# Performance work log

Hardware: AMD Instinct MI355X
Metric: run time of the kernel (lower is better)

Reference implementation:

```python
import jax, jax.numpy as jnp
import numpy as np

N, D_IN, D, E, B = 30000, 512, 512, 300000, 4096
N_RES, N_DNN = 2, 2
EPS = 1e-5


def _ln(x, g, b):
    mu = jnp.mean(x, axis=-1, keepdims=True)
    var = jnp.mean((x - mu) ** 2, axis=-1, keepdims=True)
    return (x - mu) * jax.lax.rsqrt(var + EPS) * g + b


def setup_inputs() -> dict:
    key = jax.random.key(0)
    ks = jax.random.split(key, 16)
    s = 1.0 / np.sqrt(D)
    inp = {
        "node_feat": jax.random.normal(ks[0], (N, D_IN), jnp.float32),
        "edge_hop0": jax.random.randint(ks[1], (2, E), 0, N, jnp.int32),
        "edge_hop1": jax.random.randint(ks[2], (2, E), 0, N, jnp.int32),
        "target_idx": jax.random.randint(ks[3], (B,), 0, N, jnp.int32),
        # node transform
        "Wt": jax.random.normal(ks[4], (D_IN, D), jnp.float32) / np.sqrt(D_IN),
        "bt": jnp.zeros((D,), jnp.float32),
        # GATConv (shared across both hops, one relation)
        "Wf": jax.random.normal(ks[5], (D, D), jnp.float32) * s,
        "bf": jnp.zeros((D,), jnp.float32),
        "w_att": jax.random.normal(ks[6], (2 * D,), jnp.float32) * s,
        "b_att": jnp.zeros((), jnp.float32),
        "gat_bias": jnp.zeros((D,), jnp.float32),
        # Res_DNN
        "Wp": jax.random.normal(ks[7], (D, D), jnp.float32) * s,
        "bp": jnp.zeros((D,), jnp.float32),
        "dnn_W": jax.random.normal(ks[8], (N_RES, N_DNN, D, D), jnp.float32) * s,
        "dnn_b": jnp.zeros((N_RES, N_DNN, D), jnp.float32),
        "dnn_g": jnp.ones((N_RES, N_DNN, D), jnp.float32),
        "dnn_beta": jnp.zeros((N_RES, N_DNN, D), jnp.float32),
        "res_g": jnp.ones((N_RES, D), jnp.float32),
        "res_beta": jnp.zeros((N_RES, D), jnp.float32),
        "Wc": jax.random.normal(ks[9], (D, 1), jnp.float32) * s,
        "bc": jnp.zeros((1,), jnp.float32),
    }
    return inp


def _gat(feat, edges, Wf, bf, w_att, b_att, gat_bias):
    # dst and src are the same node set / same features here
    h = feat @ Wf + bf                      # [N, D]
    di, si = edges[0], edges[1]             # [E], [E]
    # att(concat(dst_h, src_h)) == dst_h @ w[:D] + src_h @ w[D:] + b
    sd = h @ w_att[:D]                      # [N]
    ss = h @ w_att[D:]                      # [N]
    e = jnp.tanh(sd[di] + ss[si] + b_att)   # [E]
    # sparse softmax per destination row
    m = jax.ops.segment_max(e, di, num_segments=N)
    a = jnp.exp(e - m[di])
    denom = jax.ops.segment_sum(a, di, num_segments=N)
    alpha = a / denom[di]                   # [E]
    # sparse-mm aggregation
    out = jax.ops.segment_sum(alpha[:, None] * h[si], di, num_segments=N)
    return out + gat_bias


def reference(node_feat, edge_hop0, edge_hop1, target_idx, Wt, bt, Wf, bf,
              w_att, b_att, gat_bias, Wp, bp, dnn_W, dnn_b, dnn_g, dnn_beta,
              res_g, res_beta, Wc, bc):
    # node-type feature transform (dropout is identity at inference)
    feat = node_feat @ Wt + bt              # [N, D]
    # hops processed from last to first: hop1 then hop0
    for edges in (edge_hop1, edge_hop0):
        g = _gat(feat, edges, Wf, bf, w_att, b_att, gat_bias)
        feat = (feat + g) * 0.5             # mean of stacked [orig, gat_out]
    h = feat[target_idx]                    # [B, D]
    # Res_DNN head
    h = h @ Wp + bp
    for r in range(N_RES):
        sc = h
        for i in range(N_DNN):
            h = _ln(jnp.tanh(h @ dnn_W[r, i] + dnn_b[r, i]), dnn_g[r, i], dnn_beta[r, i])
        h = _ln(jnp.tanh(sc + h), res_g[r], res_beta[r])
    logits = h @ Wc + bc                    # [B, 1]
    return jax.nn.sigmoid(logits)
```

## Files before the change

### kernel.cpp

```cpp
#include <hip/hip_runtime.h>

#define D 512
typedef unsigned short ushort_t;
typedef __attribute__((ext_vector_type(8))) short bf16x8;
typedef __attribute__((ext_vector_type(4))) float f32x4;

static __device__ __forceinline__ ushort_t f2bf(float f) {
  unsigned u = __float_as_uint(f);
  u += 0x7fffu + ((u >> 16) & 1u);
  return (ushort_t)(u >> 16);
}
static __device__ __forceinline__ float bf2f(ushort_t h) {
  return __uint_as_float(((unsigned)h) << 16);
}

static __device__ __forceinline__ void gld_lds16(const void* g, void* lds) {
  __builtin_amdgcn_global_load_lds(
      (const __attribute__((address_space(1))) unsigned int*)g,
      (__attribute__((address_space(3))) unsigned int*)lds, 16, 0, 0);
}

__global__ __launch_bounds__(256) void pack_weight(
    const float* __restrict__ W, ushort_t* __restrict__ out, int K, int N, int nmat) {
  int i = blockIdx.x * 256 + threadIdx.x;
  const int per = K * N;
  if (i >= per * nmat) return;
  const int mat = i / per;
  const int r = i - mat * per;
  const int k = r / N, n = r - k * N;
  const int nt = n >> 4, col = n & 15, kt = k >> 5, kg = (k >> 3) & 3, j = k & 7;
  out[(size_t)mat * per + (((size_t)nt * (K >> 5) + kt) << 9) + ((kg << 4) + col) * 8 + j] =
      f2bf(W[(size_t)mat * per + r]);
}

__global__ __launch_bounds__(256) void conv_bf16_pad(
    const float* __restrict__ in, ushort_t* __restrict__ out, int M, int Mp, int K) {
  const size_t i4 = ((size_t)blockIdx.x * 256 + threadIdx.x) * 4;
  if (i4 >= (size_t)Mp * K) return;
  const int row = (int)(i4 / K);
  ushort4 o;
  if (row < M) {
    const float4 v = *reinterpret_cast<const float4*>(&in[i4]);
    o.x = f2bf(v.x); o.y = f2bf(v.y); o.z = f2bf(v.z); o.w = f2bf(v.w);
  } else {
    o.x = o.y = o.z = o.w = 0;
  }
  *reinterpret_cast<ushort4*>(&out[i4]) = o;
}

__global__ __launch_bounds__(512) void gemm_mfma(
    const ushort_t* __restrict__ A, const ushort_t* __restrict__ Bp,
    const float* __restrict__ bias, ushort_t* __restrict__ C16,
    const float* __restrict__ watt, float* __restrict__ sd_part,
    float* __restrict__ ss_part, int Mp, int N, int K) {
  __shared__ __align__(16) ushort_t As[2][8 * 512];
  __shared__ __align__(16) ushort_t Bs[2][8 * 512];
  const int nwg = gridDim.x;
  const int q = nwg >> 3, rm = nwg & 7;
  const int xcd = blockIdx.x & 7, kk = blockIdx.x >> 3;
  const int lin = (xcd < rm ? xcd * (q + 1) : rm * (q + 1) + (xcd - rm) * q) + kk;
  const int m0 = (lin >> 2) * 128;
  const int n0 = (lin & 3) * 128;
  const int tid = threadIdx.x;
  const int lane = tid & 63;
  const int wid = tid >> 6;
  const int wm = wid >> 1;
  const int wn = wid & 1;
  const int arow = lane & 15;
  const int akoff = (lane >> 4) * 8;
  const int c15 = lane & 15;
  const int rgrp = lane >> 4;
  const int kt32 = K >> 5;
  f32x4 acc[2][4] = {};

  auto stage = [&](int kt, int b) {
    const int k0 = kt * 32;
    gld_lds16(&A[(size_t)(m0 + wid * 16 + arow) * K + k0 + akoff],
              &As[b][wid * 512]);
    gld_lds16(&Bp[(((size_t)(n0 / 16 + wid) * kt32 + kt) << 9) + lane * 8],
              &Bs[b][wid * 512]);
  };

  stage(0, 0);
  __syncthreads();
  int cur = 0;
  for (int t = 0; t < kt32; ++t) {
    if (t + 1 < kt32) stage(t + 1, cur ^ 1);
    bf16x8 af[2], bfr[4];
#pragma unroll
    for (int mi = 0; mi < 2; ++mi)
      af[mi] = *reinterpret_cast<const bf16x8*>(&As[cur][(wm * 2 + mi) * 512 + lane * 8]);
#pragma unroll
    for (int ni = 0; ni < 4; ++ni)
      bfr[ni] = *reinterpret_cast<const bf16x8*>(&Bs[cur][(wn * 4 + ni) * 512 + lane * 8]);
#pragma unroll
    for (int mi = 0; mi < 2; ++mi)
#pragma unroll
      for (int ni = 0; ni < 4; ++ni)
        acc[mi][ni] = __builtin_amdgcn_mfma_f32_16x16x32_bf16(af[mi], bfr[ni], acc[mi][ni], 0, 0, 0);
    __syncthreads();
    cur ^= 1;
  }
  const int band = (n0 >> 6) + wn;
#pragma unroll
  for (int mi = 0; mi < 2; ++mi) {
    const int row = m0 + wm * 32 + mi * 16 + (rgrp << 2);
#pragma unroll
    for (int r = 0; r < 4; ++r) {
      float psd = 0.f, pss = 0.f;
#pragma unroll
      for (int ni = 0; ni < 4; ++ni) {
        const int col = n0 + wn * 64 + ni * 16 + c15;
        const float v = acc[mi][ni][r] + bias[col];
        C16[(size_t)(row + r) * N + col] = f2bf(v);
        if (watt) {
          psd += v * watt[col];
          pss += v * watt[D + col];
        }
      }
      if (watt) {
#pragma unroll
        for (int off = 8; off > 0; off >>= 1) {
          psd += __shfl_xor(psd, off);
          pss += __shfl_xor(pss, off);
        }
        if (c15 == 0) {
          sd_part[(size_t)band * Mp + row + r] = psd;
          ss_part[(size_t)band * Mp + row + r] = pss;
        }
      }
    }
  }
}

__global__ __launch_bounds__(256) void combine_dots(
    const float* __restrict__ sd_part, const float* __restrict__ ss_part,
    float* __restrict__ sd, float* __restrict__ ss, int Mp, int Nn) {
  const int i = blockIdx.x * 256 + threadIdx.x;
  if (i >= Nn) return;
  float a = 0.f, b = 0.f;
#pragma unroll
  for (int bnd = 0; bnd < 8; ++bnd) {
    a += sd_part[(size_t)bnd * Mp + i];
    b += ss_part[(size_t)bnd * Mp + i];
  }
  sd[i] = a;
  ss[i] = b;
}

__global__ void fill_bucket(const int* __restrict__ e1, const int* __restrict__ e0,
                            int* __restrict__ cnt, int* __restrict__ bucket,
                            int Nn, int E) {
  const int e = blockIdx.x * blockDim.x + threadIdx.x;
  if (e >= E) return;
  const int d1 = e1[e];
  const int p1 = atomicAdd(&cnt[d1], 1);
  if (p1 < 64) bucket[(size_t)d1 * 64 + p1] = e1[E + e];
  const int d0 = e0[e];
  const int p0 = atomicAdd(&cnt[Nn + d0], 1);
  if (p0 < 64) bucket[((size_t)(Nn + d0)) * 64 + p0] = e0[E + e];
}

__global__ __launch_bounds__(256) void gat_aggregate_w(
    ushort_t* __restrict__ featb, const ushort_t* __restrict__ hb,
    const float* __restrict__ sd, const float* __restrict__ ss,
    const int* __restrict__ di, const int* __restrict__ si,
    const float* __restrict__ b_att_p, const float* __restrict__ gat_bias,
    const int* __restrict__ cnt, const int* __restrict__ bucket, int Nn, int E) {
  const int dst = blockIdx.x * 4 + (threadIdx.x >> 6);
  const int lane = threadIdx.x & 63;
  if (dst >= Nn) return;
  const int deg = cnt[dst];
  const float sdd = sd[dst];
  const float ba = b_att_p[0];
  const size_t o = (size_t)dst * D + lane * 8;
  bf16x8 fv = *reinterpret_cast<const bf16x8*>(&featb[o]);
  float acc[8] = {};
  if (deg <= 64) {
    const bool valid = lane < deg;
    const int slane = valid ? bucket[(size_t)dst * 64 + lane] : 0;
    const float e = valid ? tanhf(sdd + ss[slane] + ba) : -1e30f;
    float m = e;
#pragma unroll
    for (int off = 32; off > 0; off >>= 1) m = fmaxf(m, __shfl_xor(m, off));
    const float a = valid ? expf(e - m) : 0.f;
    float s = a;
#pragma unroll
    for (int off = 32; off > 0; off >>= 1) s += __shfl_xor(s, off);
    const float w = a * ((s > 0.f) ? 1.f / s : 0.f);
    int k = 0;
    for (; k + 3 < deg; k += 4) {
      const float w0 = __shfl(w, k), w1 = __shfl(w, k + 1);
      const float w2 = __shfl(w, k + 2), w3 = __shfl(w, k + 3);
      const int s0 = __shfl(slane, k), s1 = __shfl(slane, k + 1);
      const int s2 = __shfl(slane, k + 2), s3 = __shfl(slane, k + 3);
      const bf16x8 h0 = *reinterpret_cast<const bf16x8*>(&hb[(size_t)s0 * D + lane * 8]);
      const bf16x8 h1 = *reinterpret_cast<const bf16x8*>(&hb[(size_t)s1 * D + lane * 8]);
      const bf16x8 h2 = *reinterpret_cast<const bf16x8*>(&hb[(size_t)s2 * D + lane * 8]);
      const bf16x8 h3 = *reinterpret_cast<const bf16x8*>(&hb[(size_t)s3 * D + lane * 8]);
#pragma unroll
      for (int qq = 0; qq < 8; ++qq) {
        const float t0 = w0 * bf2f((ushort_t)h0[qq]) + w1 * bf2f((ushort_t)h1[qq]);
        const float t1 = w2 * bf2f((ushort_t)h2[qq]) + w3 * bf2f((ushort_t)h3[qq]);
        acc[qq] += t0 + t1;
      }
    }
    for (; k < deg; ++k) {
      const float wk = __shfl(w, k);
      const int sk = __shfl(slane, k);
      const bf16x8 h0 = *reinterpret_cast<const bf16x8*>(&hb[(size_t)sk * D + lane * 8]);
#pragma unroll
      for (int qq = 0; qq < 8; ++qq) acc[qq] += wk * bf2f((ushort_t)h0[qq]);
    }
  } else {
    float m = -1e30f;
    for (int e = lane; e < E; e += 64)
      if (di[e] == dst) m = fmaxf(m, tanhf(sdd + ss[si[e]] + ba));
#pragma unroll
    for (int off = 32; off > 0; off >>= 1) m = fmaxf(m, __shfl_xor(m, off));
    float s = 0.f;
    for (int e = lane; e < E; e += 64)
      if (di[e] == dst) s += expf(tanhf(sdd + ss[si[e]] + ba) - m);
#pragma unroll
    for (int off = 32; off > 0; off >>= 1) s += __shfl_xor(s, off);
    const float inv = (s > 0.f) ? 1.f / s : 0.f;
    for (int base = 0; base < E; base += 64) {
      const int e = base + lane;
      const bool hit = (e < E) && (di[e] == dst);
      unsigned long long mask = __ballot(hit);
      const int sidx = hit ? si[e] : 0;
      const float aval = hit ? expf(tanhf(sdd + ss[sidx] + ba) - m) * inv : 0.f;
      while (mask) {
        const int l = __ffsll((long long)mask) - 1;
        mask &= mask - 1;
        const float wv = __shfl(aval, l);
        const int sk = __shfl(sidx, l);
        const bf16x8 hv = *reinterpret_cast<const bf16x8*>(&hb[(size_t)sk * D + lane * 8]);
#pragma unroll
        for (int qq = 0; qq < 8; ++qq) acc[qq] += wv * bf2f((ushort_t)hv[qq]);
      }
    }
  }
#pragma unroll
  for (int q = 0; q < 8; ++q) {
    const float f = (bf2f((ushort_t)fv[q]) + acc[q] + gat_bias[lane * 8 + q]) * 0.5f;
    fv[q] = (short)f2bf(f);
  }
  *reinterpret_cast<bf16x8*>(&featb[o]) = fv;
}

__global__ __launch_bounds__(1024, 4) void head_fused(
    const ushort_t* __restrict__ featb, const int* __restrict__ tidx,
    const ushort_t* __restrict__ pWp, const float* __restrict__ bp,
    const ushort_t* __restrict__ pDW, const float* __restrict__ dnn_b,
    const float* __restrict__ dnn_g, const float* __restrict__ dnn_be,
    const float* __restrict__ res_g, const float* __restrict__ res_be,
    const float* __restrict__ Wc, const float* __restrict__ bc,
    float* __restrict__ out) {
  __shared__ __align__(16) ushort_t A_lds[16 * 512];
  __shared__ float lsum[16][16], lsq[16][16], meanv[16], rsv[16];
  const int tid = threadIdx.x;
  const int lane = tid & 63;
  const int wave = tid >> 6;
  const int nt0 = wave * 2;
  const int c15 = lane & 15;
  const int rgrp = lane >> 4;

  {
    const int row = tid >> 6, col8 = tid & 63;
    const int g = tidx[blockIdx.x * 16 + row];
    const bf16x8 v = *reinterpret_cast<const bf16x8*>(&featb[(size_t)g * D + col8 * 8]);
    *reinterpret_cast<bf16x8*>(&A_lds[row * 512 + (col8 ^ (row & 7)) * 8]) = v;
  }
  __syncthreads();

  auto do_gemm = [&](const ushort_t* __restrict__ W, f32x4& a0, f32x4& a1) {
    a0 = f32x4{0.f, 0.f, 0.f, 0.f};
    a1 = f32x4{0.f, 0.f, 0.f, 0.f};
    bf16x8 c0 = *reinterpret_cast<const bf16x8*>(
        &W[(((size_t)nt0 * 16 + 0) << 9) + lane * 8]);
    bf16x8 c1 = *reinterpret_cast<const bf16x8*>(
        &W[(((size_t)(nt0 + 1) * 16 + 0) << 9) + lane * 8]);
#pragma unroll
    for (int kt = 0; kt < 16; ++kt) {
      bf16x8 n0 = c0, n1 = c1;
      if (kt < 15) {
        n0 = *reinterpret_cast<const bf16x8*>(
            &W[(((size_t)nt0 * 16 + kt + 1) << 9) + lane * 8]);
        n1 = *reinterpret_cast<const bf16x8*>(
            &W[(((size_t)(nt0 + 1) * 16 + kt + 1) << 9) + lane * 8]);
      }
      const int col8 = kt * 4 + rgrp;
      const bf16x8 af = *reinterpret_cast<const bf16x8*>(
          &A_lds[c15 * 512 + (col8 ^ (c15 & 7)) * 8]);
      a0 = __builtin_amdgcn_mfma_f32_16x16x32_bf16(af, c0, a0, 0, 0, 0);
      a1 = __builtin_amdgcn_mfma_f32_16x16x32_bf16(af, c1, a1, 0, 0, 0);
      c0 = n0;
      c1 = n1;
    }
  };

  auto block_ln = [&](f32x4& v0, f32x4& v1, const float* __restrict__ g,
                      const float* __restrict__ be) {
    float psum[4], psq[4];
#pragma unroll
    for (int r = 0; r < 4; ++r) {
      psum[r] = v0[r] + v1[r];
      psq[r] = v0[r] * v0[r] + v1[r] * v1[r];
    }
#pragma unroll
    for (int off = 8; off > 0; off >>= 1)
#pragma unroll
      for (int r = 0; r < 4; ++r) {
        psum[r] += __shfl_xor(psum[r], off);
        psq[r] += __shfl_xor(psq[r], off);
      }
    if (c15 == 0) {
#pragma unroll
      for (int r = 0; r < 4; ++r) {
        lsum[wave][rgrp * 4 + r] = psum[r];
        lsq[wave][rgrp * 4 + r] = psq[r];
      }
    }
    __syncthreads();
    if (tid < 16) {
      float s = 0.f, qq = 0.f;
#pragma unroll
      for (int w = 0; w < 16; ++w) { s += lsum[w][tid]; qq += lsq[w][tid]; }
      const float mean = s * (1.f / 512.f);
      const float var = qq * (1.f / 512.f) - mean * mean;
      meanv[tid] = mean;
      rsv[tid] = rsqrtf(var + 1e-5f);
    }
    __syncthreads();
    const int col0 = nt0 * 16 + c15;
    const int col1 = (nt0 + 1) * 16 + c15;
    const float g0 = g[col0], b0 = be[col0];
    const float g1 = g[col1], b1 = be[col1];
#pragma unroll
    for (int r = 0; r < 4; ++r) {
      const int row = rgrp * 4 + r;
      v0[r] = (v0[r] - meanv[row]) * rsv[row] * g0 + b0;
      v1[r] = (v1[r] - meanv[row]) * rsv[row] * g1 + b1;
    }
  };

  auto store_A = [&](const f32x4& v0, const f32x4& v1) {
    const int col0 = nt0 * 16 + c15;
    const int col1 = (nt0 + 1) * 16 + c15;
#pragma unroll
    for (int r = 0; r < 4; ++r) {
      const int row = rgrp * 4 + r;
      A_lds[row * 512 + (((col0 >> 3) ^ (row & 7)) << 3) + (col0 & 7)] = f2bf(v0[r]);
      A_lds[row * 512 + (((col1 >> 3) ^ (row & 7)) << 3) + (col1 & 7)] = f2bf(v1[r]);
    }
  };

  f32x4 sc0, sc1, acc0, acc1, ln0, ln1;

  do_gemm(pWp, acc0, acc1);
  {
    const float bv0 = bp[nt0 * 16 + c15];
    const float bv1 = bp[(nt0 + 1) * 16 + c15];
#pragma unroll
    for (int r = 0; r < 4; ++r) { sc0[r] = acc0[r] + bv0; sc1[r] = acc1[r] + bv1; }
  }
  __syncthreads();
  store_A(sc0, sc1);
  __syncthreads();

  for (int rb = 0; rb < 2; ++rb) {
    {
      const int st = rb * 2;
      do_gemm(pDW + (size_t)st * D * D, acc0, acc1);
      const float bv0 = dnn_b[st * D + nt0 * 16 + c15];
      const float bv1 = dnn_b[st * D + (nt0 + 1) * 16 + c15];
#pragma unroll
      for (int r = 0; r < 4; ++r) {
        acc0[r] = tanhf(acc0[r] + bv0);
        acc1[r] = tanhf(acc1[r] + bv1);
      }
      block_ln(acc0, acc1, dnn_g + st * D, dnn_be + st * D);
      store_A(acc0, acc1);
      __syncthreads();
    }
    {
      const int st = rb * 2 + 1;
      do_gemm(pDW + (size_t)st * D * D, ln0, ln1);
      const float bv0 = dnn_b[st * D + nt0 * 16 + c15];
      const float bv1 = dnn_b[st * D + (nt0 + 1) * 16 + c15];
#pragma unroll
      for (int r = 0; r < 4; ++r) {
        ln0[r] = tanhf(ln0[r] + bv0);
        ln1[r] = tanhf(ln1[r] + bv1);
      }
      block_ln(ln0, ln1, dnn_g + st * D, dnn_be + st * D);
    }
#pragma unroll
    for (int r = 0; r < 4; ++r) {
      acc0[r] = tanhf(sc0[r] + ln0[r]);
      acc1[r] = tanhf(sc1[r] + ln1[r]);
    }
    block_ln(acc0, acc1, res_g + rb * D, res_be + rb * D);
    sc0 = acc0;
    sc1 = acc1;
    if (rb == 0) {
      store_A(sc0, sc1);
      __syncthreads();
    }
  }

  float pr[4];
  {
    const float w0 = Wc[nt0 * 16 + c15];
    const float w1 = Wc[(nt0 + 1) * 16 + c15];
#pragma unroll
    for (int r = 0; r < 4; ++r) pr[r] = sc0[r] * w0 + sc1[r] * w1;
  }
#pragma unroll
  for (int off = 8; off > 0; off >>= 1)
#pragma unroll
    for (int r = 0; r < 4; ++r) pr[r] += __shfl_xor(pr[r], off);
  __syncthreads();
  if (c15 == 0) {
#pragma unroll
    for (int r = 0; r < 4; ++r) lsum[wave][rgrp * 4 + r] = pr[r];
  }
  __syncthreads();
  if (tid < 16) {
    float s = 0.f;
#pragma unroll
    for (int w = 0; w < 16; ++w) s += lsum[w][tid];
    out[blockIdx.x * 16 + tid] = 1.f / (1.f + expf(-(s + bc[0])));
  }
}

extern "C" void kernel_launch(void* const* d_in, const int* in_sizes, int n_in,
                              void* d_out, int out_size, void* d_ws, size_t ws_size,
                              hipStream_t stream) {
  (void)n_in; (void)out_size; (void)ws_size;
  const float* node_feat = (const float*)d_in[0];
  const int* edge0 = (const int*)d_in[1];
  const int* edge1 = (const int*)d_in[2];
  const int* tidx = (const int*)d_in[3];
  const float* Wt = (const float*)d_in[4];
  const float* bt = (const float*)d_in[5];
  const float* Wf = (const float*)d_in[6];
  const float* bfp = (const float*)d_in[7];
  const float* w_att = (const float*)d_in[8];
  const float* b_att = (const float*)d_in[9];
  const float* gat_bias = (const float*)d_in[10];
  const float* Wp = (const float*)d_in[11];
  const float* bp = (const float*)d_in[12];
  const float* dnn_W = (const float*)d_in[13];
  const float* dnn_b = (const float*)d_in[14];
  const float* dnn_g = (const float*)d_in[15];
  const float* dnn_be = (const float*)d_in[16];
  const float* res_g = (const float*)d_in[17];
  const float* res_be = (const float*)d_in[18];
  const float* Wc = (const float*)d_in[19];
  const float* bc = (const float*)d_in[20];
  float* out = (float*)d_out;

  const int Nn = in_sizes[0] / D;
  const int E = in_sizes[1] / 2;
  const int B = in_sizes[3];
  const int K_IN = in_sizes[4] / D;
  const int Mp = (Nn + 127) / 128 * 128;
  const int N2 = 2 * Nn;

  char* p = (char*)d_ws;
  auto alloc = [&](size_t bytes) -> char* {
    char* r = p;
    p += (bytes + 255) & ~(size_t)255;
    return r;
  };
  ushort_t* featb = (ushort_t*)alloc((size_t)Mp * D * 2);
  ushort_t* hb = (ushort_t*)alloc((size_t)Mp * D * 2);
  float* sd = (float*)alloc((size_t)Nn * 4);
  float* ss = (float*)alloc((size_t)Nn * 4);
  float* sd_part = (float*)alloc((size_t)8 * Mp * 4);
  float* ss_part = (float*)alloc((size_t)8 * Mp * 4);
  int* cnt = (int*)alloc((size_t)N2 * 4);
  int* bucket = (int*)alloc((size_t)N2 * 64 * 4);
  ushort_t* pWt = (ushort_t*)alloc((size_t)K_IN * D * 2);
  ushort_t* pWf = (ushort_t*)alloc((size_t)D * D * 2);
  ushort_t* pWp = (ushort_t*)alloc((size_t)D * D * 2);
  ushort_t* pDWall = (ushort_t*)alloc((size_t)4 * D * D * 2);

  dim3 blk(256);
  const int nw4 = (Nn + 3) / 4;

  {
    pack_weight<<<(K_IN * D + 255) / 256, blk, 0, stream>>>(Wt, pWt, K_IN, D, 1);
    pack_weight<<<(D * D + 255) / 256, blk, 0, stream>>>(Wf, pWf, D, D, 1);
    pack_weight<<<(D * D + 255) / 256, blk, 0, stream>>>(Wp, pWp, D, D, 1);
    pack_weight<<<(4 * D * D + 255) / 256, blk, 0, stream>>>(dnn_W, pDWall, D, D, 4);
    conv_bf16_pad<<<((size_t)Mp * K_IN / 4 + 255) / 256, blk, 0, stream>>>(
        node_feat, hb , Nn, Mp, K_IN);
  }

  hipMemsetAsync(cnt, 0, (size_t)N2 * 4, stream);
  fill_bucket<<<(E + 255) / 256, blk, 0, stream>>>(edge1, edge0, cnt, bucket, Nn, E);

  gemm_mfma<<<dim3(4 * (Mp / 128)), dim3(512), 0, stream>>>(
      hb, pWt, bt, featb, nullptr, nullptr, nullptr, Mp, D, K_IN);

  const int* hops[2] = {edge1, edge0};
  for (int hp = 0; hp < 2; ++hp) {
    gemm_mfma<<<dim3(4 * (Mp / 128)), dim3(512), 0, stream>>>(
        featb, pWf, bfp, hb, w_att, sd_part, ss_part, Mp, D, D);
    combine_dots<<<(Nn + 255) / 256, blk, 0, stream>>>(sd_part, ss_part, sd, ss, Mp, Nn);
    gat_aggregate_w<<<nw4, blk, 0, stream>>>(
        featb, hb, sd, ss, hops[hp], hops[hp] + E, b_att, gat_bias,
        cnt + hp * Nn, bucket + (size_t)hp * Nn * 64, Nn, E);
  }

  head_fused<<<B / 16, dim3(1024), 0, stream>>>(
      featb, tidx, pWp, bp, pDWall, dnn_b, dnn_g, dnn_be, res_g, res_be,
      Wc, bc, out);
}
```

Baseline: 342.9 us.

## Restrict GAT aggregation to nodes reachable from target indices

Marks the target nodes and their hop-0 source neighbours, then compacts them into index lists. The hop-1 aggregation runs only for nodes the hop-0 stage will read, and the hop-0 aggregation runs only for the target rows. This is meant to cut aggregation work that never reaches the output. It costs extra flagging and compaction kernels with atomics, and the per-row order becomes scattered. The four weight-packing launches and the memset are also folded into single kernels to reduce launch overhead.

```diff
diff --git a/kernel.cpp b/kernel.cpp
--- a/kernel.cpp
+++ b/kernel.cpp
@@ -20,17 +20,24 @@
       (__attribute__((address_space(3))) unsigned int*)lds, 16, 0, 0);
 }
 
-__global__ __launch_bounds__(256) void pack_weight(
-    const float* __restrict__ W, ushort_t* __restrict__ out, int K, int N, int nmat) {
+__global__ __launch_bounds__(256) void pack_weight7(
+    const float* __restrict__ Wt, const float* __restrict__ Wf,
+    const float* __restrict__ Wp, const float* __restrict__ Wd,
+    ushort_t* __restrict__ out) {
+  const int per = D * D;
   int i = blockIdx.x * 256 + threadIdx.x;
-  const int per = K * N;
-  if (i >= per * nmat) return;
+  if (i >= per * 7) return;
   const int mat = i / per;
   const int r = i - mat * per;
-  const int k = r / N, n = r - k * N;
+  const float* W;
+  if (mat == 0) W = Wt;
+  else if (mat == 1) W = Wf;
+  else if (mat == 2) W = Wp;
+  else W = Wd + (size_t)(mat - 3) * per;
+  const int k = r / D, n = r - k * D;
   const int nt = n >> 4, col = n & 15, kt = k >> 5, kg = (k >> 3) & 3, j = k & 7;
-  out[(size_t)mat * per + (((size_t)nt * (K >> 5) + kt) << 9) + ((kg << 4) + col) * 8 + j] =
-      f2bf(W[(size_t)mat * per + r]);
+  out[(size_t)mat * per + (((size_t)nt * (D >> 5) + kt) << 9) + ((kg << 4) + col) * 8 + j] =
+      f2bf(W[r]);
 }
 
 __global__ __launch_bounds__(256) void conv_bf16_pad(
@@ -46,6 +53,46 @@
     o.x = o.y = o.z = o.w = 0;
   }
   *reinterpret_cast<ushort4*>(&out[i4]) = o;
+}
+
+__global__ __launch_bounds__(256) void init_buffers(
+    int* __restrict__ cnt, int* __restrict__ tflag, int* __restrict__ nflag,
+    int* __restrict__ counters, int Nn, int N2) {
+  const int i = blockIdx.x * 256 + threadIdx.x;
+  if (i < N2) cnt[i] = 0;
+  if (i < Nn) { tflag[i] = 0; nflag[i] = 0; }
+  if (i < 2) counters[i * 64] = 0;
+}
+
+__global__ void fill_bucket(const int* __restrict__ e1, const int* __restrict__ e0,
+                            const int* __restrict__ tidx, int* __restrict__ tflag,
+                            int* __restrict__ cnt, int* __restrict__ bucket,
+                            int Nn, int E, int B) {
+  const int e = blockIdx.x * blockDim.x + threadIdx.x;
+  if (e < B) tflag[tidx[e]] = 1;
+  if (e >= E) return;
+  const int d1 = e1[e];
+  const int p1 = atomicAdd(&cnt[d1], 1);
+  if (p1 < 64) bucket[(size_t)d1 * 64 + p1] = e1[E + e];
+  const int d0 = e0[e];
+  const int p0 = atomicAdd(&cnt[Nn + d0], 1);
+  if (p0 < 64) bucket[((size_t)(Nn + d0)) * 64 + p0] = e0[E + e];
+}
+
+__global__ void flag_srcs(const int* __restrict__ e0, const int* __restrict__ tflag,
+                          int* __restrict__ nflag, int E) {
+  const int e = blockIdx.x * blockDim.x + threadIdx.x;
+  if (e < E && tflag[e0[e]]) nflag[e0[E + e]] = 1;
+}
+
+__global__ void compact2(const int* __restrict__ tflag, const int* __restrict__ nflag,
+                         int* __restrict__ tlist, int* __restrict__ nlist,
+                         int* __restrict__ counters, int Nn) {
+  const int i = blockIdx.x * 256 + threadIdx.x;
+  if (i >= Nn) return;
+  const int tf = tflag[i];
+  if (tf) tlist[atomicAdd(&counters[0], 1)] = i;
+  if (tf | nflag[i]) nlist[atomicAdd(&counters[64], 1)] = i;
 }
 
 __global__ __launch_bounds__(512) void gemm_mfma(
@@ -148,28 +195,18 @@
   ss[i] = b;
 }
 
-__global__ void fill_bucket(const int* __restrict__ e1, const int* __restrict__ e0,
-                            int* __restrict__ cnt, int* __restrict__ bucket,
-                            int Nn, int E) {
-  const int e = blockIdx.x * blockDim.x + threadIdx.x;
-  if (e >= E) return;
-  const int d1 = e1[e];
-  const int p1 = atomicAdd(&cnt[d1], 1);
-  if (p1 < 64) bucket[(size_t)d1 * 64 + p1] = e1[E + e];
-  const int d0 = e0[e];
-  const int p0 = atomicAdd(&cnt[Nn + d0], 1);
-  if (p0 < 64) bucket[((size_t)(Nn + d0)) * 64 + p0] = e0[E + e];
-}
-
 __global__ __launch_bounds__(256) void gat_aggregate_w(
     ushort_t* __restrict__ featb, const ushort_t* __restrict__ hb,
     const float* __restrict__ sd, const float* __restrict__ ss,
     const int* __restrict__ di, const int* __restrict__ si,
     const float* __restrict__ b_att_p, const float* __restrict__ gat_bias,
-    const int* __restrict__ cnt, const int* __restrict__ bucket, int Nn, int E) {
-  const int dst = blockIdx.x * 4 + (threadIdx.x >> 6);
+    const int* __restrict__ cnt, const int* __restrict__ bucket,
+    const int* __restrict__ dstlist, const int* __restrict__ dcount,
+    int Nn, int E) {
+  const int gidx = blockIdx.x * 4 + (threadIdx.x >> 6);
   const int lane = threadIdx.x & 63;
-  if (dst >= Nn) return;
+  if (gidx >= *dcount) return;
+  const int dst = dstlist[gidx];
   const int deg = cnt[dst];
   const float sdd = sd[dst];
   const float ba = b_att_p[0];
@@ -483,25 +520,29 @@
   float* ss_part = (float*)alloc((size_t)8 * Mp * 4);
   int* cnt = (int*)alloc((size_t)N2 * 4);
   int* bucket = (int*)alloc((size_t)N2 * 64 * 4);
-  ushort_t* pWt = (ushort_t*)alloc((size_t)K_IN * D * 2);
-  ushort_t* pWf = (ushort_t*)alloc((size_t)D * D * 2);
-  ushort_t* pWp = (ushort_t*)alloc((size_t)D * D * 2);
-  ushort_t* pDWall = (ushort_t*)alloc((size_t)4 * D * D * 2);
+  int* tflag = (int*)alloc((size_t)Nn * 4);
+  int* nflag = (int*)alloc((size_t)Nn * 4);
+  int* tlist = (int*)alloc((size_t)B * 4);
+  int* nlist = (int*)alloc((size_t)Nn * 4);
+  int* counters = (int*)alloc(512);
+  ushort_t* pAll = (ushort_t*)alloc((size_t)7 * D * D * 2);
+  ushort_t* pWt = pAll;
+  ushort_t* pWf = pAll + (size_t)D * D;
+  ushort_t* pWp = pAll + (size_t)2 * D * D;
+  ushort_t* pDWall = pAll + (size_t)3 * D * D;
 
   dim3 blk(256);
-  const int nw4 = (Nn + 3) / 4;
-
-  {
-    pack_weight<<<(K_IN * D + 255) / 256, blk, 0, stream>>>(Wt, pWt, K_IN, D, 1);
-    pack_weight<<<(D * D + 255) / 256, blk, 0, stream>>>(Wf, pWf, D, D, 1);
-    pack_weight<<<(D * D + 255) / 256, blk, 0, stream>>>(Wp, pWp, D, D, 1);
-    pack_weight<<<(4 * D * D + 255) / 256, blk, 0, stream>>>(dnn_W, pDWall, D, D, 4);
-    conv_bf16_pad<<<((size_t)Mp * K_IN / 4 + 255) / 256, blk, 0, stream>>>(
-        node_feat, hb , Nn, Mp, K_IN);
-  }
-
-  hipMemsetAsync(cnt, 0, (size_t)N2 * 4, stream);
-  fill_bucket<<<(E + 255) / 256, blk, 0, stream>>>(edge1, edge0, cnt, bucket, Nn, E);
+
+  pack_weight7<<<(7 * D * D + 255) / 256, blk, 0, stream>>>(Wt, Wf, Wp, dnn_W, pAll);
+  conv_bf16_pad<<<((size_t)Mp * K_IN / 4 + 255) / 256, blk, 0, stream>>>(
+      node_feat, hb , Nn, Mp, K_IN);
+
+  init_buffers<<<(N2 + 255) / 256, blk, 0, stream>>>(cnt, tflag, nflag, counters, Nn, N2);
+  fill_bucket<<<(E + 255) / 256, blk, 0, stream>>>(edge1, edge0, tidx, tflag,
+                                                   cnt, bucket, Nn, E, B);
+  flag_srcs<<<(E + 255) / 256, blk, 0, stream>>>(edge0, tflag, nflag, E);
+  compact2<<<(Nn + 255) / 256, blk, 0, stream>>>(tflag, nflag, tlist, nlist,
+                                                 counters, Nn);
 
   gemm_mfma<<<dim3(4 * (Mp / 128)), dim3(512), 0, stream>>>(
       hb, pWt, bt, featb, nullptr, nullptr, nullptr, Mp, D, K_IN);
@@ -511,9 +552,15 @@
     gemm_mfma<<<dim3(4 * (Mp / 128)), dim3(512), 0, stream>>>(
         featb, pWf, bfp, hb, w_att, sd_part, ss_part, Mp, D, D);
     combine_dots<<<(Nn + 255) / 256, blk, 0, stream>>>(sd_part, ss_part, sd, ss, Mp, Nn);
-    gat_aggregate_w<<<nw4, blk, 0, stream>>>(
-        featb, hb, sd, ss, hops[hp], hops[hp] + E, b_att, gat_bias,
-        cnt + hp * Nn, bucket + (size_t)hp * Nn * 64, Nn, E);
+    if (hp == 0) {
+      gat_aggregate_w<<<(Nn + 3) / 4, blk, 0, stream>>>(
+          featb, hb, sd, ss, hops[hp], hops[hp] + E, b_att, gat_bias,
+          cnt + hp * Nn, bucket + (size_t)hp * Nn * 64, nlist, &counters[64], Nn, E);
+    } else {
+      gat_aggregate_w<<<(B + 3) / 4, blk, 0, stream>>>(
+          featb, hb, sd, ss, hops[hp], hops[hp] + E, b_att, gat_bias,
+          cnt + hp * Nn, bucket + (size_t)hp * Nn * 64, tlist, &counters[0], Nn, E);
+    }
   }
 
   head_fused<<<B / 16, dim3(1024), 0, stream>>>(
```

Measured after the change: 297.5 us. 1.15x faster.
